# Optimization experiments

Measured on AMD Instinct MI355X. Metric: run time of the kernel, lower is better.

## Reference

```python
import jax, jax.numpy as jnp
import numpy as np

N_NODES = 100000


def _gcn_norm(edge_index, num_nodes):
    # PyG gcn_norm with add_self_loops=True, edge_weight=1:
    # A_hat = A + I; norm_e = deg^{-1/2}[src] * deg^{-1/2}[dst]
    loop = jnp.arange(num_nodes, dtype=edge_index.dtype)
    src = jnp.concatenate([edge_index[0], loop])
    dst = jnp.concatenate([edge_index[1], loop])
    deg = jax.ops.segment_sum(jnp.ones_like(src, dtype=jnp.float32), dst,
                              num_segments=num_nodes)
    dinv = jnp.where(deg > 0, jax.lax.rsqrt(deg), 0.0)
    norm = dinv[src] * dinv[dst]  # [E + N]
    return src, dst, norm


def _gcn_conv(x, src, dst, norm, W, b, num_nodes):
    h = x @ W                                  # [N, out] dense GEMM
    msg = h[src] * norm[:, None]               # gather + scale per edge
    out = jax.ops.segment_sum(msg, dst, num_segments=num_nodes)
    return out + b


def setup_inputs() -> dict:
    key = jax.random.key(0)
    k1, k2, k3, k4, k5, k6 = jax.random.split(key, 6)
    in_c, hid_c, out_c = 128, 128, 64
    E = 3200000
    x = jax.random.normal(k1, (N_NODES, in_c), dtype=jnp.float32)
    edge_index = jax.random.randint(k2, (2, E), 0, N_NODES, dtype=jnp.int64)
    # Glorot-style init for GCNConv linear weights, zero bias (PyG default)
    W1 = jax.random.normal(k3, (in_c, hid_c), dtype=jnp.float32) / np.sqrt(in_c)
    b1 = jnp.zeros((hid_c,), dtype=jnp.float32)
    W2 = jax.random.normal(k4, (hid_c, out_c), dtype=jnp.float32) / np.sqrt(hid_c)
    b2 = jnp.zeros((out_c,), dtype=jnp.float32)
    return {"x": x, "edge_index": edge_index, "W1": W1, "b1": b1,
            "W2": W2, "b2": b2}


def reference(x, edge_index, W1, b1, W2, b2):
    # Dropout is identity in eval mode (F.dropout(training=False)).
    src, dst, norm = _gcn_norm(edge_index, N_NODES)
    h = _gcn_conv(x, src, dst, norm, W1, b1, N_NODES)
    out = _gcn_conv(h, src, dst, norm, W2, b2, N_NODES)
    return out
```

## Files before the change

kernel.cpp:

```cpp
#include <hip/hip_runtime.h>
#include <hip/hip_fp16.h>
#include <cstdint>
#include <cstddef>


#define NB    391
#define BSH   8
#define CAPS  32
#define PBLK  512
#define OVCAP 4096
#define CAPB  9216

typedef _Float16 half8 __attribute__((ext_vector_type(8)));
typedef float    floatx4 __attribute__((ext_vector_type(4)));
typedef unsigned uint4v  __attribute__((ext_vector_type(4)));


__global__ __launch_bounds__(256) void partition_k(
    const int* __restrict__ src, const int* __restrict__ dst,
    int* __restrict__ ovcur, unsigned* __restrict__ ovrecs,
    unsigned* __restrict__ tailbuf, int* __restrict__ tailcnt, int E) {
    __shared__ unsigned stag[NB][CAPS + 1];
    __shared__ int scnt[NB];
    const int t = threadIdx.x;
    for (int i = t; i < NB; i += 256) scnt[i] = 0;
    __syncthreads();

    const int Q = E >> 2;
    const int per = (Q + PBLK - 1) / PBLK;
    const int qbeg = blockIdx.x * per;
    const int qend = min(qbeg + per, Q);
    const int4* src4 = (const int4*)src;
    const int4* dst4 = (const int4*)dst;

    for (int q = qbeg + t; q < qend; q += 256) {
        const int4 s4 = src4[q];
        const int4 d4 = dst4[q];
#pragma unroll
        for (int j = 0; j < 4; ++j) {
            const int s = (&s4.x)[j], d = (&d4.x)[j];
            const int b = d >> BSH;
            const unsigned rec = ((unsigned)(d & 255) << 17) | (unsigned)s;
            const int slot = atomicAdd(&scnt[b], 1);
            if (slot < CAPS) stag[b][slot] = rec;
            else { const int p = atomicAdd(&ovcur[b], 1); ovrecs[(size_t)b * OVCAP + p] = rec; }
        }
    }
    if (blockIdx.x == 0) {
        for (int e = (E & ~3) + t; e < E; e += 256) {
            const int s = src[e], d = dst[e];
            const int b = d >> BSH;
            const unsigned rec = ((unsigned)(d & 255) << 17) | (unsigned)s;
            const int slot = atomicAdd(&scnt[b], 1);
            if (slot < CAPS) stag[b][slot] = rec;
            else { const int p = atomicAdd(&ovcur[b], 1); ovrecs[(size_t)b * OVCAP + p] = rec; }
        }
    }
    __syncthreads();

    for (int i = t; i < NB * CAPS; i += 256) {
        const int b = i >> 5, j = i & 31;
        if (j < min(scnt[b], CAPS))
            tailbuf[((size_t)b * PBLK + blockIdx.x) * CAPS + j] = stag[b][j];
    }
    for (int b = t; b < NB; b += 256)
        tailcnt[blockIdx.x * NB + b] = min(scnt[b], CAPS);
}

__global__ __launch_bounds__(256) void build_w12_k(
    const unsigned* __restrict__ ovrecs, const int* __restrict__ ovcur,
    const unsigned* __restrict__ tailbuf, const int* __restrict__ tailcnt,
    int* __restrict__ rbeg, int* __restrict__ rend,
    int* __restrict__ csr, float* __restrict__ dinv,
    const float* __restrict__ W1, const float* __restrict__ W2,
    const float* __restrict__ b1, _Float16* __restrict__ BhiT,
    _Float16* __restrict__ BloT, float* __restrict__ c2, int N) {
    __shared__ int tcs[PBLK];
    __shared__ int soff[PBLK];
    __shared__ int sseg[256];
    __shared__ unsigned lrec[CAPB];
    __shared__ int cnt[256];
    __shared__ int scan[256];
    __shared__ int lpos[256];
    __shared__ int tcum_sh;
    const int t = threadIdx.x, b = blockIdx.x;

    if (b >= NB) {
        const int bb = b - NB;
        if (bb < 32) {
            const int r = bb * 4 + (t >> 6);
            const int c = t & 63;
            float acc = 0.f;
            for (int k = 0; k < 128; ++k) acc += W1[r * 128 + k] * W2[k * 64 + c];
            const _Float16 h = (_Float16)acc;
            BhiT[c * 128 + r] = h;
            BloT[c * 128 + r] = (_Float16)(acc - (float)h);
        } else if (t < 64) {
            float acc = 0.f;
            for (int k = 0; k < 128; ++k) acc += b1[k] * W2[k * 64 + t];
            c2[t] = acc;
        }
        return;
    }

    const int n0 = b << BSH;
    const int nn = min(256, N - n0);
    const int gbase = b * CAPB;
    const size_t tb0 = (size_t)b * PBLK * CAPS;
    const int ov = ovcur[b];

    for (int i = t; i < PBLK; i += 256) tcs[i] = tailcnt[i * NB + b];
    cnt[t] = 0;
    __syncthreads();

    const int a0 = tcs[2 * t], a1 = tcs[2 * t + 1];
    sseg[t] = a0 + a1;
    __syncthreads();
    for (int o = 1; o < 256; o <<= 1) {
        int x = (t >= o) ? sseg[t - o] : 0;
        __syncthreads(); sseg[t] += x; __syncthreads();
    }
    const int ex2 = sseg[t] - (a0 + a1);
    soff[2 * t] = ex2;
    soff[2 * t + 1] = ex2 + a0;
    if (t == 255) tcum_sh = sseg[255];
    __syncthreads();
    const int tcum = tcum_sh;

    for (int i = t; i < PBLK * CAPS; i += 256) {
        const int seg = i >> 5, j = i & 31;
        if (j < tcs[seg]) lrec[soff[seg] + j] = tailbuf[tb0 + i];
    }
    for (int i = t; i < ov; i += 256) lrec[tcum + i] = ovrecs[(size_t)b * OVCAP + i];
    __syncthreads();

    const int tot = tcum + ov;
    for (int i = t; i < tot; i += 256) atomicAdd(&cnt[lrec[i] >> 17], 1);
    __syncthreads();

    scan[t] = cnt[t];
    __syncthreads();
    for (int o = 1; o < 256; o <<= 1) {
        int x = (t >= o) ? scan[t - o] : 0;
        __syncthreads(); scan[t] += x; __syncthreads();
    }
    const int excl = scan[t] - cnt[t];
    lpos[t] = excl;
    if (t < nn) {
        rbeg[n0 + t] = gbase + excl;
        rend[n0 + t] = gbase + scan[t];
        dinv[n0 + t] = rsqrtf((float)(cnt[t] + 1));
    }
    __syncthreads();

    for (int i = t; i < tot; i += 256) {
        const unsigned r = lrec[i];
        const int pq = atomicAdd(&lpos[r >> 17], 1);
        csr[gbase + pq] = (int)(r & 0x1FFFFu);
    }
}

__global__ __launch_bounds__(256) void gemm_mfma_k(
    const float* __restrict__ X, const _Float16* __restrict__ BhiT,
    const _Float16* __restrict__ BloT, const float* __restrict__ dinv,
    __half* __restrict__ g, int N) {
    const int t = threadIdx.x;
    const int wave = t >> 6, lane = t & 63;
    const int m16 = lane & 15;
    const int quad = lane >> 4;
    const int rowbase = blockIdx.x * 64 + wave * 16;
    const int arow = min(rowbase + m16, N - 1);

    floatx4 acc[4] = {{0.f,0.f,0.f,0.f},{0.f,0.f,0.f,0.f},
                      {0.f,0.f,0.f,0.f},{0.f,0.f,0.f,0.f}};

#pragma unroll
    for (int ks = 0; ks < 4; ++ks) {
        const int k0 = ks * 32 + quad * 8;
        const float4 xa = *(const float4*)(X + (size_t)arow * 128 + k0);
        const float4 xb = *(const float4*)(X + (size_t)arow * 128 + k0 + 4);
        const float xs[8] = {xa.x, xa.y, xa.z, xa.w, xb.x, xb.y, xb.z, xb.w};
        half8 ahi, alo;
#pragma unroll
        for (int j = 0; j < 8; ++j) {
            const _Float16 h = (_Float16)xs[j];
            ahi[j] = h;
            alo[j] = (_Float16)(xs[j] - (float)h);
        }
#pragma unroll
        for (int c = 0; c < 4; ++c) {
            const int n = c * 16 + m16;
            const half8 bhi = *(const half8*)(BhiT + n * 128 + k0);
            const half8 blo = *(const half8*)(BloT + n * 128 + k0);
            acc[c] = __builtin_amdgcn_mfma_f32_16x16x32_f16(ahi, bhi, acc[c], 0, 0, 0);
            acc[c] = __builtin_amdgcn_mfma_f32_16x16x32_f16(ahi, blo, acc[c], 0, 0, 0);
            acc[c] = __builtin_amdgcn_mfma_f32_16x16x32_f16(alo, bhi, acc[c], 0, 0, 0);
        }
    }

#pragma unroll
    for (int r = 0; r < 4; ++r) {
        const int grow = rowbase + quad * 4 + r;
        if (grow < N) {
            const float di = dinv[grow];
#pragma unroll
            for (int c = 0; c < 4; ++c)
                g[(size_t)grow * 64 + c * 16 + m16] = __float2half(acc[c][r] * di);
        }
    }
}

template <int PASS2>
__global__ __launch_bounds__(256) void agg_k(
    const __half* __restrict__ gin, const int* __restrict__ rbeg,
    const int* __restrict__ rend, const int* __restrict__ csr,
    const float* __restrict__ dinv, void* __restrict__ outp,
    float* __restrict__ p, const float* __restrict__ c2,
    const float* __restrict__ b2, int N) {
    const int wv = (blockIdx.x * 256 + threadIdx.x) >> 6;
    const int lane = threadIdx.x & 63;
    const int half = lane >> 5;
    const int d = wv * 2 + half;
    if (d >= N) return;
    const int w    = lane & 7;
    const int slot = (lane >> 3) & 3;
    const int beg = rbeg[d], end = rend[d];
    const float di = dinv[d];
    const half8* __restrict__ grow = (const half8*)gin;

    const half8 vself = grow[((size_t)d << 3) + w];

    float acc[8];
#pragma unroll
    for (int q = 0; q < 8; ++q) acc[q] = 0.f;
    float accp = (!PASS2 && slot == 0) ? di : 0.f;

    auto accum = [&](half8 f) {
        const uint4v u = __builtin_bit_cast(uint4v, f);
#pragma unroll
        for (int q = 0; q < 4; ++q) {
            asm("v_fma_mix_f32 %0, %1, 1.0, %0 op_sel:[0,0,0] op_sel_hi:[1,0,0]"
                : "+v"(acc[2 * q]) : "v"(u[q]));
            asm("v_fma_mix_f32 %0, %1, 1.0, %0 op_sel:[1,0,0] op_sel_hi:[1,0,0]"
                : "+v"(acc[2 * q + 1]) : "v"(u[q]));
        }
    };

    int e = beg + slot;
    while (e + 12 < end) {
        const int s0 = csr[e], s1 = csr[e + 4], s2 = csr[e + 8], s3 = csr[e + 12];
        const half8 f0 = grow[((size_t)s0 << 3) + w];
        const half8 f1 = grow[((size_t)s1 << 3) + w];
        const half8 f2 = grow[((size_t)s2 << 3) + w];
        const half8 f3 = grow[((size_t)s3 << 3) + w];
        if (!PASS2) accp += dinv[s0] + dinv[s1] + dinv[s2] + dinv[s3];
        accum(f0); accum(f1); accum(f2); accum(f3);
        e += 16;
    }
    if (e + 4 < end) {
        const int s0 = csr[e], s1 = csr[e + 4];
        const half8 f0 = grow[((size_t)s0 << 3) + w];
        const half8 f1 = grow[((size_t)s1 << 3) + w];
        if (!PASS2) accp += dinv[s0] + dinv[s1];
        accum(f0); accum(f1);
        e += 8;
    }
    while (e < end) {
        const int s0 = csr[e];
        const half8 f0 = grow[((size_t)s0 << 3) + w];
        if (!PASS2) accp += dinv[s0];
        accum(f0);
        e += 4;
    }

#pragma unroll
    for (int m = 8; m <= 16; m <<= 1) {
#pragma unroll
        for (int q = 0; q < 8; ++q) acc[q] += __shfl_xor(acc[q], m);
        if (!PASS2) accp += __shfl_xor(accp, m);
    }

    if (slot == 0) {
        const __half2* sh2 = (const __half2*)&vself;
#pragma unroll
        for (int q = 0; q < 4; ++q) {
            const float2 t2 = __half22float2(sh2[q]);
            acc[2 * q]     += t2.x;
            acc[2 * q + 1] += t2.y;
        }
        if (PASS2) {
            const float pd = p[d];
            float o[8];
#pragma unroll
            for (int q = 0; q < 8; ++q)
                o[q] = acc[q] * di + pd * c2[w * 8 + q] + b2[w * 8 + q];
            float4* op = (float4*)outp + ((size_t)d << 4) + w * 2;
            op[0] = make_float4(o[0], o[1], o[2], o[3]);
            op[1] = make_float4(o[4], o[5], o[6], o[7]);
        } else {
            const float sc = di * di;
            half8 ov;
#pragma unroll
            for (int q = 0; q < 8; ++q) ov[q] = (_Float16)(acc[q] * sc);
            ((half8*)outp)[((size_t)d << 3) + w] = ov;
            if ((lane & 31) == 0) p[d] = di * accp;
        }
    }
}

extern "C" void kernel_launch(void* const* d_in, const int* in_sizes, int n_in,
                              void* d_out, int out_size, void* d_ws, size_t ws_size,
                              hipStream_t stream) {
    const float* x  = (const float*)d_in[0];
    const int*   ei = (const int*)d_in[1];
    const float* W1 = (const float*)d_in[2];
    const float* b1 = (const float*)d_in[3];
    const float* W2 = (const float*)d_in[4];
    const float* b2 = (const float*)d_in[5];
    float* out = (float*)d_out;

    const int N = in_sizes[0] / 128;
    const int E = in_sizes[1] / 2;
    const int* src = ei;
    const int* dst = ei + E;

    char* ws = (char*)d_ws;
    auto take = [&](size_t bytes) { char* q = ws; ws += (bytes + 255) & ~(size_t)255; return q; };
    int*      ovcur   = (int*)     take(NB * 4);
    int*      rbeg    = (int*)     take((size_t)N * 4);
    int*      rendp   = (int*)     take((size_t)N * 4);
    float*    dinv    = (float*)   take((size_t)N * 4);
    float*    pbuf    = (float*)   take((size_t)N * 4);
    _Float16* BhiT    = (_Float16*)take(128 * 64 * 2);
    _Float16* BloT    = (_Float16*)take(128 * 64 * 2);
    float*    c2      = (float*)   take(64 * 4);
    int*      tailcnt = (int*)     take((size_t)NB * PBLK * 4);
    unsigned* ovrecs  = (unsigned*)take((size_t)NB * OVCAP * 4);
    unsigned* tailbuf = (unsigned*)take((size_t)NB * PBLK * CAPS * 4);
    int*      csr     = (int*)     take((size_t)NB * CAPB * 4);
    __half*   g       = (__half*)  take((size_t)N * 64 * 2);
    __half*   t1      = (__half*)  take((size_t)N * 64 * 2);

    hipMemsetAsync(ovcur, 0, NB * 4, stream);

    partition_k<<<PBLK, 256, 0, stream>>>(src, dst, ovcur, ovrecs, tailbuf, tailcnt, E);
    build_w12_k<<<NB + 33, 256, 0, stream>>>(ovrecs, ovcur, tailbuf, tailcnt,
                                             rbeg, rendp, csr, dinv,
                                             W1, W2, b1, BhiT, BloT, c2, N);
    gemm_mfma_k<<<(N + 63) / 64, 256, 0, stream>>>(x, BhiT, BloT, dinv, g, N);

    const int aggBlocks = (N + 7) / 8;
    agg_k<0><<<aggBlocks, 256, 0, stream>>>(g,  rbeg, rendp, csr, dinv, t1,  pbuf, c2, b2, N);
    agg_k<1><<<aggBlocks, 256, 0, stream>>>(t1, rbeg, rendp, csr, dinv, out, pbuf, c2, b2, N);
}
```

Baseline: 297.8 us.

## Fuse partition and CSR build into one cooperative kernel with finer buckets

Merges the edge partition kernel and the CSR build/weight-fold kernel into a single cooperative launch separated by a grid-wide sync. This removes the memset and one kernel launch. Buckets are halved to 128 nodes (782 buckets, 16-slot staging) so the shared staging fits a union with the build state. Global per-bucket overflow atomics are replaced by per-block 64-bit overflow lists, which every bucket task must scan across all 512 blocks. That scan adds redundant global reads, and records beyond the 256-per-block overflow cap are silently dropped.

```diff
diff --git a/kernel.cpp b/kernel.cpp
--- a/kernel.cpp
+++ b/kernel.cpp
@@ -1,162 +1,197 @@
 #include <hip/hip_runtime.h>
 #include <hip/hip_fp16.h>
+#include <hip/hip_cooperative_groups.h>
 #include <cstdint>
 #include <cstddef>
 
 
-#define NB    391
-#define BSH   8
-#define CAPS  32
 #define PBLK  512
-#define OVCAP 4096
-#define CAPB  9216
+#define BSH2  7
+#define NB2   782
+#define CAPS2 16
+#define OVB   256
+#define CAPB2 4736
+#define LRECC (CAPB2 + 64)
 
 typedef _Float16 half8 __attribute__((ext_vector_type(8)));
 typedef float    floatx4 __attribute__((ext_vector_type(4)));
 typedef unsigned uint4v  __attribute__((ext_vector_type(4)));
 
 
-__global__ __launch_bounds__(256) void partition_k(
+struct PartS {
+    unsigned stag[NB2][CAPS2 + 1];
+    int scnt[NB2];
+    int ovn;
+};
+struct BuildS {
+    int tcs[PBLK];
+    int soff[PBLK];
+    int sseg[256];
+    unsigned lrec[LRECC];
+    int cnt[256];
+    int scan[256];
+    int lpos[256];
+    int tcum;
+    int ovn;
+};
+
+__global__ __launch_bounds__(256) void part_build_w12_k(
     const int* __restrict__ src, const int* __restrict__ dst,
-    int* __restrict__ ovcur, unsigned* __restrict__ ovrecs,
-    unsigned* __restrict__ tailbuf, int* __restrict__ tailcnt, int E) {
-    __shared__ unsigned stag[NB][CAPS + 1];
-    __shared__ int scnt[NB];
-    const int t = threadIdx.x;
-    for (int i = t; i < NB; i += 256) scnt[i] = 0;
-    __syncthreads();
-
-    const int Q = E >> 2;
-    const int per = (Q + PBLK - 1) / PBLK;
-    const int qbeg = blockIdx.x * per;
-    const int qend = min(qbeg + per, Q);
-    const int4* src4 = (const int4*)src;
-    const int4* dst4 = (const int4*)dst;
-
-    for (int q = qbeg + t; q < qend; q += 256) {
-        const int4 s4 = src4[q];
-        const int4 d4 = dst4[q];
-#pragma unroll
-        for (int j = 0; j < 4; ++j) {
-            const int s = (&s4.x)[j], d = (&d4.x)[j];
-            const int b = d >> BSH;
-            const unsigned rec = ((unsigned)(d & 255) << 17) | (unsigned)s;
-            const int slot = atomicAdd(&scnt[b], 1);
-            if (slot < CAPS) stag[b][slot] = rec;
-            else { const int p = atomicAdd(&ovcur[b], 1); ovrecs[(size_t)b * OVCAP + p] = rec; }
-        }
-    }
-    if (blockIdx.x == 0) {
-        for (int e = (E & ~3) + t; e < E; e += 256) {
-            const int s = src[e], d = dst[e];
-            const int b = d >> BSH;
-            const unsigned rec = ((unsigned)(d & 255) << 17) | (unsigned)s;
-            const int slot = atomicAdd(&scnt[b], 1);
-            if (slot < CAPS) stag[b][slot] = rec;
-            else { const int p = atomicAdd(&ovcur[b], 1); ovrecs[(size_t)b * OVCAP + p] = rec; }
-        }
-    }
-    __syncthreads();
-
-    for (int i = t; i < NB * CAPS; i += 256) {
-        const int b = i >> 5, j = i & 31;
-        if (j < min(scnt[b], CAPS))
-            tailbuf[((size_t)b * PBLK + blockIdx.x) * CAPS + j] = stag[b][j];
-    }
-    for (int b = t; b < NB; b += 256)
-        tailcnt[blockIdx.x * NB + b] = min(scnt[b], CAPS);
-}
-
-__global__ __launch_bounds__(256) void build_w12_k(
-    const unsigned* __restrict__ ovrecs, const int* __restrict__ ovcur,
-    const unsigned* __restrict__ tailbuf, const int* __restrict__ tailcnt,
+    unsigned long long* __restrict__ ov64, int* __restrict__ ovcnt,
+    unsigned* __restrict__ tailbuf, int* __restrict__ tailcnt,
     int* __restrict__ rbeg, int* __restrict__ rend,
     int* __restrict__ csr, float* __restrict__ dinv,
     const float* __restrict__ W1, const float* __restrict__ W2,
     const float* __restrict__ b1, _Float16* __restrict__ BhiT,
-    _Float16* __restrict__ BloT, float* __restrict__ c2, int N) {
-    __shared__ int tcs[PBLK];
-    __shared__ int soff[PBLK];
-    __shared__ int sseg[256];
-    __shared__ unsigned lrec[CAPB];
-    __shared__ int cnt[256];
-    __shared__ int scan[256];
-    __shared__ int lpos[256];
-    __shared__ int tcum_sh;
-    const int t = threadIdx.x, b = blockIdx.x;
-
-    if (b >= NB) {
-        const int bb = b - NB;
-        if (bb < 32) {
-            const int r = bb * 4 + (t >> 6);
-            const int c = t & 63;
-            float acc = 0.f;
-            for (int k = 0; k < 128; ++k) acc += W1[r * 128 + k] * W2[k * 64 + c];
-            const _Float16 h = (_Float16)acc;
-            BhiT[c * 128 + r] = h;
-            BloT[c * 128 + r] = (_Float16)(acc - (float)h);
-        } else if (t < 64) {
-            float acc = 0.f;
-            for (int k = 0; k < 128; ++k) acc += b1[k] * W2[k * 64 + t];
-            c2[t] = acc;
-        }
-        return;
-    }
-
-    const int n0 = b << BSH;
-    const int nn = min(256, N - n0);
-    const int gbase = b * CAPB;
-    const size_t tb0 = (size_t)b * PBLK * CAPS;
-    const int ov = ovcur[b];
-
-    for (int i = t; i < PBLK; i += 256) tcs[i] = tailcnt[i * NB + b];
-    cnt[t] = 0;
+    _Float16* __restrict__ BloT, float* __restrict__ c2,
+    int E, int N)
+{
+    __shared__ union { PartS p; BuildS b; } sh;
+    const int t = threadIdx.x, bid = blockIdx.x;
+
+    for (int i = t; i < NB2; i += 256) sh.p.scnt[i] = 0;
+    if (t == 0) sh.p.ovn = 0;
     __syncthreads();
 
-    const int a0 = tcs[2 * t], a1 = tcs[2 * t + 1];
-    sseg[t] = a0 + a1;
+    const int Q = E >> 2;
+    const int per = (Q + PBLK - 1) / PBLK;
+    const int qbeg = bid * per;
+    const int qend = min(qbeg + per, Q);
+    const int4* src4 = (const int4*)src;
+    const int4* dst4 = (const int4*)dst;
+
+    for (int q = qbeg + t; q < qend; q += 256) {
+        const int4 s4 = src4[q];
+        const int4 d4 = dst4[q];
+#pragma unroll
+        for (int j = 0; j < 4; ++j) {
+            const int s = (&s4.x)[j], d = (&d4.x)[j];
+            const int b = d >> BSH2;
+            const unsigned rec = ((unsigned)(d & 127) << 17) | (unsigned)s;
+            const int slot = atomicAdd(&sh.p.scnt[b], 1);
+            if (slot < CAPS2) sh.p.stag[b][slot] = rec;
+            else {
+                const int pos = atomicAdd(&sh.p.ovn, 1);
+                if (pos < OVB)
+                    ov64[(size_t)bid * OVB + pos] =
+                        ((unsigned long long)(unsigned)d << 17) | (unsigned)s;
+            }
+        }
+    }
+    if (bid == 0) {
+        for (int e = (E & ~3) + t; e < E; e += 256) {
+            const int s = src[e], d = dst[e];
+            const int b = d >> BSH2;
+            const unsigned rec = ((unsigned)(d & 127) << 17) | (unsigned)s;
+            const int slot = atomicAdd(&sh.p.scnt[b], 1);
+            if (slot < CAPS2) sh.p.stag[b][slot] = rec;
+            else {
+                const int pos = atomicAdd(&sh.p.ovn, 1);
+                if (pos < OVB)
+                    ov64[(size_t)bid * OVB + pos] =
+                        ((unsigned long long)(unsigned)d << 17) | (unsigned)s;
+            }
+        }
+    }
     __syncthreads();
-    for (int o = 1; o < 256; o <<= 1) {
-        int x = (t >= o) ? sseg[t - o] : 0;
-        __syncthreads(); sseg[t] += x; __syncthreads();
-    }
-    const int ex2 = sseg[t] - (a0 + a1);
-    soff[2 * t] = ex2;
-    soff[2 * t + 1] = ex2 + a0;
-    if (t == 255) tcum_sh = sseg[255];
-    __syncthreads();
-    const int tcum = tcum_sh;
-
-    for (int i = t; i < PBLK * CAPS; i += 256) {
-        const int seg = i >> 5, j = i & 31;
-        if (j < tcs[seg]) lrec[soff[seg] + j] = tailbuf[tb0 + i];
-    }
-    for (int i = t; i < ov; i += 256) lrec[tcum + i] = ovrecs[(size_t)b * OVCAP + i];
-    __syncthreads();
-
-    const int tot = tcum + ov;
-    for (int i = t; i < tot; i += 256) atomicAdd(&cnt[lrec[i] >> 17], 1);
-    __syncthreads();
-
-    scan[t] = cnt[t];
-    __syncthreads();
-    for (int o = 1; o < 256; o <<= 1) {
-        int x = (t >= o) ? scan[t - o] : 0;
-        __syncthreads(); scan[t] += x; __syncthreads();
-    }
-    const int excl = scan[t] - cnt[t];
-    lpos[t] = excl;
-    if (t < nn) {
-        rbeg[n0 + t] = gbase + excl;
-        rend[n0 + t] = gbase + scan[t];
-        dinv[n0 + t] = rsqrtf((float)(cnt[t] + 1));
-    }
-    __syncthreads();
-
-    for (int i = t; i < tot; i += 256) {
-        const unsigned r = lrec[i];
-        const int pq = atomicAdd(&lpos[r >> 17], 1);
-        csr[gbase + pq] = (int)(r & 0x1FFFFu);
+
+    for (int i = t; i < NB2 * CAPS2; i += 256) {
+        const int b = i >> 4, j = i & 15;
+        if (j < min(sh.p.scnt[b], CAPS2))
+            tailbuf[((size_t)b * PBLK + bid) * CAPS2 + j] = sh.p.stag[b][j];
+    }
+    for (int b = t; b < NB2; b += 256)
+        tailcnt[bid * NB2 + b] = min(sh.p.scnt[b], CAPS2);
+    if (t == 0) ovcnt[bid] = min(sh.p.ovn, OVB);
+
+    cooperative_groups::this_grid().sync();
+
+    for (int task = bid; task < NB2 + 33; task += PBLK) {
+        if (task < NB2) {
+            const int b = task;
+            const int n0 = b << BSH2;
+            const int nn = min(128, N - n0);
+            const int gbase = b * CAPB2;
+            const size_t tb0 = (size_t)b * PBLK * CAPS2;
+
+            for (int i = t; i < PBLK; i += 256) sh.b.tcs[i] = tailcnt[i * NB2 + b];
+            sh.b.cnt[t] = 0;
+            if (t == 0) sh.b.ovn = 0;
+            __syncthreads();
+
+            const int a0 = sh.b.tcs[2 * t], a1 = sh.b.tcs[2 * t + 1];
+            sh.b.sseg[t] = a0 + a1;
+            __syncthreads();
+            for (int o = 1; o < 256; o <<= 1) {
+                int x = (t >= o) ? sh.b.sseg[t - o] : 0;
+                __syncthreads(); sh.b.sseg[t] += x; __syncthreads();
+            }
+            const int ex2 = sh.b.sseg[t] - (a0 + a1);
+            sh.b.soff[2 * t] = ex2;
+            sh.b.soff[2 * t + 1] = ex2 + a0;
+            if (t == 255) sh.b.tcum = sh.b.sseg[255];
+            __syncthreads();
+            const int tcum = sh.b.tcum;
+
+            for (int i = t; i < PBLK * CAPS2; i += 256) {
+                const int seg = i >> 4, j = i & 15;
+                if (j < sh.b.tcs[seg]) sh.b.lrec[sh.b.soff[seg] + j] = tailbuf[tb0 + i];
+            }
+            for (int blk = t; blk < PBLK; blk += 256) {
+                const int c = ovcnt[blk];
+                for (int i2 = 0; i2 < c; ++i2) {
+                    const unsigned long long r = ov64[(size_t)blk * OVB + i2];
+                    const int dd = (int)(r >> 17);
+                    if ((dd >> BSH2) == b) {
+                        const int pos = atomicAdd(&sh.b.ovn, 1);
+                        sh.b.lrec[tcum + pos] =
+                            ((unsigned)(dd & 127) << 17) | (unsigned)(r & 0x1FFFFu);
+                    }
+                }
+            }
+            __syncthreads();
+
+            const int tot = tcum + sh.b.ovn;
+            for (int i = t; i < tot; i += 256) atomicAdd(&sh.b.cnt[sh.b.lrec[i] >> 17], 1);
+            __syncthreads();
+
+            sh.b.scan[t] = sh.b.cnt[t];
+            __syncthreads();
+            for (int o = 1; o < 256; o <<= 1) {
+                int x = (t >= o) ? sh.b.scan[t - o] : 0;
+                __syncthreads(); sh.b.scan[t] += x; __syncthreads();
+            }
+            const int excl = sh.b.scan[t] - sh.b.cnt[t];
+            sh.b.lpos[t] = excl;
+            if (t < nn) {
+                rbeg[n0 + t] = gbase + excl;
+                rend[n0 + t] = gbase + sh.b.scan[t];
+                dinv[n0 + t] = rsqrtf((float)(sh.b.cnt[t] + 1));
+            }
+            __syncthreads();
+
+            for (int i = t; i < tot; i += 256) {
+                const unsigned r = sh.b.lrec[i];
+                const int pq = atomicAdd(&sh.b.lpos[r >> 17], 1);
+                csr[gbase + pq] = (int)(r & 0x1FFFFu);
+            }
+        } else {
+            const int bb = task - NB2;
+            if (bb < 32) {
+                const int r = bb * 4 + (t >> 6);
+                const int c = t & 63;
+                float acc = 0.f;
+                for (int k = 0; k < 128; ++k) acc += W1[r * 128 + k] * W2[k * 64 + c];
+                const _Float16 h = (_Float16)acc;
+                BhiT[c * 128 + r] = h;
+                BloT[c * 128 + r] = (_Float16)(acc - (float)h);
+            } else if (t < 64) {
+                float acc = 0.f;
+                for (int k = 0; k < 128; ++k) acc += b1[k] * W2[k * 64 + t];
+                c2[t] = acc;
+            }
+        }
+        __syncthreads();
     }
 }
 
@@ -321,12 +356,11 @@
 
     const int N = in_sizes[0] / 128;
     const int E = in_sizes[1] / 2;
-    const int* src = ei;
-    const int* dst = ei + E;
+    const int* srcp = ei;
+    const int* dstp = ei + E;
 
     char* ws = (char*)d_ws;
     auto take = [&](size_t bytes) { char* q = ws; ws += (bytes + 255) & ~(size_t)255; return q; };
-    int*      ovcur   = (int*)     take(NB * 4);
     int*      rbeg    = (int*)     take((size_t)N * 4);
     int*      rendp   = (int*)     take((size_t)N * 4);
     float*    dinv    = (float*)   take((size_t)N * 4);
@@ -334,19 +368,24 @@
     _Float16* BhiT    = (_Float16*)take(128 * 64 * 2);
     _Float16* BloT    = (_Float16*)take(128 * 64 * 2);
     float*    c2      = (float*)   take(64 * 4);
-    int*      tailcnt = (int*)     take((size_t)NB * PBLK * 4);
-    unsigned* ovrecs  = (unsigned*)take((size_t)NB * OVCAP * 4);
-    unsigned* tailbuf = (unsigned*)take((size_t)NB * PBLK * CAPS * 4);
-    int*      csr     = (int*)     take((size_t)NB * CAPB * 4);
+    int*      ovcnt   = (int*)     take((size_t)PBLK * 4);
+    unsigned long long* ov64 = (unsigned long long*)take((size_t)PBLK * OVB * 8);
+    int*      tailcnt = (int*)     take((size_t)PBLK * NB2 * 4);
+    unsigned* tailbuf = (unsigned*)take((size_t)NB2 * PBLK * CAPS2 * 4);
+    int*      csr     = (int*)     take((size_t)NB2 * CAPB2 * 4);
     __half*   g       = (__half*)  take((size_t)N * 64 * 2);
     __half*   t1      = (__half*)  take((size_t)N * 64 * 2);
 
-    hipMemsetAsync(ovcur, 0, NB * 4, stream);
-
-    partition_k<<<PBLK, 256, 0, stream>>>(src, dst, ovcur, ovrecs, tailbuf, tailcnt, E);
-    build_w12_k<<<NB + 33, 256, 0, stream>>>(ovrecs, ovcur, tailbuf, tailcnt,
-                                             rbeg, rendp, csr, dinv,
-                                             W1, W2, b1, BhiT, BloT, c2, N);
+    int E_ = E, N_ = N;
+    void* kargs[] = {
+        (void*)&srcp, (void*)&dstp, (void*)&ov64, (void*)&ovcnt,
+        (void*)&tailbuf, (void*)&tailcnt, (void*)&rbeg, (void*)&rendp,
+        (void*)&csr, (void*)&dinv, (void*)&W1, (void*)&W2, (void*)&b1,
+        (void*)&BhiT, (void*)&BloT, (void*)&c2, (void*)&E_, (void*)&N_
+    };
+    hipLaunchCooperativeKernel((void*)part_build_w12_k, dim3(PBLK), dim3(256),
+                               kargs, 0, stream);
+
     gemm_mfma_k<<<(N + 63) / 64, 256, 0, stream>>>(x, BhiT, BloT, dinv, g, N);
 
     const int aggBlocks = (N + 7) / 8;
```

Result: slower. 377.7 us (+26.8%).
